# Optimization experiments

Measured on AMD Instinct MI355X. Metric: run time of the kernel, lower is better.

The kernel has to match this reference:

```python
import jax, jax.numpy as jnp
import numpy as np

ND, ED, HD, L, K = 128, 64, 256, 4, 24   # node_dim, edge_dim(num_rbf), hidden_dim, num_layers, max_neighbors
CUTOFF = 8.0
N = 2048  # n_atoms


def _silu(x):
    return x * jax.nn.sigmoid(x)


def _lattice(lengths, angles):
    a, b, c = lengths[0], lengths[1], lengths[2]
    deg = jnp.asarray(np.pi / 180.0, lengths.dtype)
    al, be, ga = angles[0] * deg, angles[1] * deg, angles[2] * deg
    lx = a
    xy = b * jnp.cos(ga)
    xz = c * jnp.cos(be)
    ly = b * jnp.sin(ga)
    yz = (b * c * jnp.cos(al) - xy * xz) / ly
    lz = jnp.sqrt(c ** 2 - xz ** 2 - yz ** 2)
    z = jnp.zeros((), lengths.dtype)
    return jnp.stack([jnp.stack([lx, z, z]), jnp.stack([xy, ly, z]), jnp.stack([xz, yz, lz])])


def _rbf(d):
    centers = jnp.linspace(0.0, CUTOFF, ED)
    widths = jnp.full((ED,), CUTOFF / ED)
    d = d[..., None]
    g = jnp.exp(-(d - centers) ** 2 / (2.0 * widths ** 2))
    cv = 0.5 * (jnp.cos(d * jnp.pi / CUTOFF) + 1.0) * (d < CUTOFF).astype(d.dtype)
    return g * cv


def _forward(atom_types, frac_coords, lengths, angles, timesteps, emb, tW, tb,
             eW1, eb1, eW2, eb2, nW1, nb1, nW2, nb2, cW1, cb1, cW2, cb2):
    n = frac_coords.shape[0]
    lattice = _lattice(lengths, angles)            # [3,3]
    cart = frac_coords @ lattice                   # [n,3]

    # ---- vectorized periodic neighbor graph (replaces host triple loop) ----
    shifts = jnp.asarray(np.array([[i, j, k] for i in (-1, 0, 1) for j in (-1, 0, 1) for k in (-1, 0, 1)],
                                  dtype=np.float32))
    sv = shifts @ lattice                          # [27,3]
    p = cart[None, :, :] + sv[:, None, :]          # [27,n,3] shifted atom positions
    # squared distances without materializing [27,n,n,3]
    d2 = (p * p).sum(-1)[:, :, None] + (cart * cart).sum(-1)[None, None, :] \
         - 2.0 * jnp.einsum('snk,mk->snm', p, cart)      # [27, n_j, n_i]
    dist = jnp.sqrt(jnp.maximum(d2, 1e-12))
    cand = jnp.where((dist < CUTOFF) & (dist > 0.01), dist, jnp.inf)
    cand = cand.reshape(27 * n, n).T               # [n_i, 27*n_j]; flat f = s*n + j
    _, idx = jax.lax.top_k(-cand, K)               # K smallest distances per atom i
    d_k = jnp.take_along_axis(cand, idx, axis=1)   # [n,K]
    dst = (idx % n).reshape(-1)                    # neighbor atom j (edge_list = [i, j])
    src = jnp.repeat(jnp.arange(n), K)             # center atom i
    valid = jnp.isfinite(d_k).reshape(-1)
    m = valid.astype(jnp.float32)[:, None]         # [E,1] pad mask
    d_e = jnp.where(valid, d_k.reshape(-1), 0.0)
    edge_attr = _rbf(d_e)                          # [E, ED]

    # ---- EGNN stack ----
    nf = emb[atom_types] + timesteps @ tW + tb     # [n, ND]
    coords = cart
    seg = lambda x, i: jax.ops.segment_sum(x, i, num_segments=n)
    for l in range(L):
        ef = jnp.concatenate([nf[src], nf[dst], edge_attr], axis=-1)   # [E, 2*ND+ED]
        msg = _silu(_silu(ef @ eW1[l] + eb1[l]) @ eW2[l] + eb2[l])     # [E, HD]
        aggr = seg(msg * m, dst)                                       # [n, HD]
        nf = nf + _silu(jnp.concatenate([nf, aggr], axis=-1) @ nW1[l] + nb1[l]) @ nW2[l] + nb2[l]
        w = _silu(msg @ cW1[l] + cb1[l]) @ cW2[l] + cb2[l]             # [E,1]
        cd = coords[src] - coords[dst]
        cd = cd / (jnp.linalg.norm(cd, axis=-1, keepdims=True) + 1e-8)
        coords = coords + seg(w * cd * m, dst)
    return nf, coords


def setup_inputs() -> dict:
    key = jax.random.key(0)
    ks = jax.random.split(key, 16)
    pr = lambda k, shape: jax.random.normal(k, shape, jnp.float32) * 0.02
    return dict(
        atom_types=jax.random.randint(ks[0], (N,), 0, 100),
        frac_coords=jax.random.uniform(ks[1], (N, 3), jnp.float32),
        lengths=jnp.ones((3,), jnp.float32) * 12.0,
        angles=jnp.ones((3,), jnp.float32) * 90.0,
        timesteps=jax.random.normal(ks[2], (N, 128), jnp.float32),
        emb=pr(ks[3], (100, ND)),
        tW=pr(ks[4], (128, ND)), tb=jnp.zeros((ND,), jnp.float32),
        eW1=pr(ks[5], (L, 2 * ND + ED, HD)), eb1=jnp.zeros((L, HD), jnp.float32),
        eW2=pr(ks[6], (L, HD, HD)), eb2=jnp.zeros((L, HD), jnp.float32),
        nW1=pr(ks[7], (L, ND + HD, HD)), nb1=jnp.zeros((L, HD), jnp.float32),
        nW2=pr(ks[8], (L, HD, ND)), nb2=jnp.zeros((L, ND), jnp.float32),
        cW1=pr(ks[9], (L, HD, HD // 2)), cb1=jnp.zeros((L, HD // 2), jnp.float32),
        cW2=pr(ks[10], (L, HD // 2, 1)), cb2=jnp.zeros((L, 1), jnp.float32),
    )


def reference(atom_types, frac_coords, lengths, angles, timesteps, emb, tW, tb,
              eW1, eb1, eW2, eb2, nW1, nb1, nW2, nb2, cW1, cb1, cW2, cb2):
    return _forward(atom_types, frac_coords, lengths, angles, timesteps, emb, tW, tb,
                    eW1, eb1, eW2, eb2, nW1, nb1, nW2, nb2, cW1, cb1, cW2, cb2)
```

## Files before the change

kernel.cpp:

```cpp
#include <hip/hip_runtime.h>
#include <math.h>

#define NA 2048
#define KN 24
#define NE (NA*KN)
#define NDIM 128
#define EDIM 64
#define HDIM 256
#define NLAYER 4
#define MAXDEG 256

typedef __attribute__((ext_vector_type(8))) short bf16x8;
typedef __attribute__((ext_vector_type(4))) float f32x4;

__device__ __forceinline__ float siluf(float x) { return x / (1.0f + expf(-x)); }
__device__ __forceinline__ ushort f2b(float x) {
    unsigned u = __float_as_uint(x);
    return (ushort)((u + 0x7fffu + ((u >> 16) & 1u)) >> 16);
}
__device__ __forceinline__ float b2f(ushort h) { return __uint_as_float(((unsigned)h) << 16); }

__device__ __forceinline__ void gl_lds(const void* g, void* lds) {
    __builtin_amdgcn_global_load_lds(
        (const __attribute__((address_space(1))) unsigned int*)g,
        (__attribute__((address_space(3))) unsigned int*)lds, 16, 0, 0);
}

struct Lat { float lx, xy, xz, ly, yz, lz; };

__device__ __forceinline__ Lat make_lattice(const float* lengths, const float* angles) {
    const float deg = 0.017453292519943295f;
    float a = lengths[0], b = lengths[1], c = lengths[2];
    float al = angles[0]*deg, be = angles[1]*deg, ga = angles[2]*deg;
    Lat L;
    L.lx = a;
    L.xy = b * cosf(ga);
    L.xz = c * cosf(be);
    L.ly = b * sinf(ga);
    L.yz = (b*c*cosf(al) - L.xy*L.xz) / L.ly;
    L.lz = sqrtf(c*c - L.xz*L.xz - L.yz*L.yz);
    return L;
}

__global__ void setup_kernel(const float* __restrict__ frac, const float* __restrict__ lengths,
                             const float* __restrict__ angles, float* __restrict__ cart,
                             float* __restrict__ cxg, float* __restrict__ cyg,
                             float* __restrict__ czg, float* __restrict__ sv) {
    int i = blockIdx.x*blockDim.x + threadIdx.x;
    Lat L = make_lattice(lengths, angles);
    if (i < NA) {
        float f0 = frac[i*3], f1 = frac[i*3+1], f2 = frac[i*3+2];
        float x = f0*L.lx + f1*L.xy + f2*L.xz;
        float y = f1*L.ly + f2*L.yz;
        float z = f2*L.lz;
        cart[i*3+0] = x; cart[i*3+1] = y; cart[i*3+2] = z;
        cxg[i] = x; cyg[i] = y; czg[i] = z;
    }
    if (i < 27) {
        float s0 = (float)(i/9 - 1), s1 = (float)((i/3)%3 - 1), s2 = (float)(i%3 - 1);
        sv[i*3+0] = s0*L.lx + s1*L.xy + s2*L.xz;
        sv[i*3+1] = s1*L.ly + s2*L.yz;
        sv[i*3+2] = s2*L.lz;
    }
}

__global__ __launch_bounds__(64) void knn_kernel(
        const float* __restrict__ cxg, const float* __restrict__ cyg,
        const float* __restrict__ czg, const float* __restrict__ lengths,
        const float* __restrict__ angles, const float* __restrict__ sv,
        int* __restrict__ dstl, ushort* __restrict__ rbf16) {
    __shared__ float sd2L[16][64];
    __shared__ int   sfL[16][64];
    const int lane = threadIdx.x;
    const int i = blockIdx.x;
    Lat L = make_lattice(lengths, angles);
    const float deg = 0.017453292519943295f;
    const bool ortho = fabsf(cosf(angles[0]*deg)) < 1e-6f &&
                       fabsf(cosf(angles[1]*deg)) < 1e-6f &&
                       fabsf(cosf(angles[2]*deg)) < 1e-6f;
    const float cx = cxg[i], cy = cyg[i], cz = czg[i];
    const float invlx = 1.0f/L.lx, invly = 1.0f/L.ly, invlz = 1.0f/L.lz;
    float R = 2.8f;
    int mycnt = 0, cnt = 0;
    bool flatm = false;
    for (int attempt = 0; attempt < 8; ++attempt) {
        const float R2 = R*R;
        mycnt = 0;
        flatm = !ortho || (attempt == 7);
        if (!flatm) {
#pragma unroll 2
            for (int j0 = 0; j0 < NA; j0 += 64) {
                const int j = j0 + lane;
                const float dx = cxg[j] - cx, dy = cyg[j] - cy, dz = czg[j] - cz;
                const float kx = rintf(dx*invlx), ky = rintf(dy*invly), kz = rintf(dz*invlz);
                const float ex = dx - (kx*L.lx + ky*L.xy + kz*L.xz);
                const float ey = dy - (ky*L.ly + kz*L.yz);
                const float ez = dz - kz*L.lz;
                const float d2 = fmaf(ex,ex,fmaf(ey,ey,ez*ez));
                if (d2 < R2 && d2 > 1e-4f) {
                    const int s = (1-(int)kx)*9 + (1-(int)ky)*3 + (1-(int)kz);
                    if (mycnt < 16) { sd2L[mycnt][lane] = d2; sfL[mycnt][lane] = (s<<11) + j; }
                    ++mycnt;
                }
            }
            if (__ballot(mycnt > 16)) {
                flatm = true;
            } else {
                int tot = mycnt;
                for (int off = 32; off > 0; off >>= 1) tot += __shfl_xor(tot, off, 64);
                cnt = tot;
            }
        }
        if (flatm) {
            cnt = 0;
            for (int s = 0; s < 27; ++s) {
                const float svx = sv[s*3], svy = sv[s*3+1], svz = sv[s*3+2];
                for (int j0 = 0; j0 < NA; j0 += 64) {
                    const int j = j0 + lane;
                    const float ex = cxg[j] + svx - cx;
                    const float ey = cyg[j] + svy - cy;
                    const float ez = czg[j] + svz - cz;
                    const float d2 = fmaf(ex,ex,fmaf(ey,ey,ez*ez));
                    const bool hit = (d2 < R2) && (d2 > 1e-4f);
                    const unsigned long long m = __ballot(hit);
                    const int rank = __popcll(m & ((1ull<<lane)-1ull));
                    const int slot = cnt + rank;
                    if (hit && slot < 1024) { sd2L[slot>>6][slot&63] = d2; sfL[slot>>6][slot&63] = (s<<11)+j; }
                    cnt += __popcll(m);
                }
            }
            cnt = min(cnt, 1024);
        }
        if (cnt >= KN) break;
        R = fminf(R*1.6f, flatm ? 8.0f : 5.9f);
    }
    int vq;
    if (flatm) vq = (lane < cnt) ? min(16, ((cnt - 1 - lane) >> 6) + 1) : 0;
    else       vq = mycnt;
    unsigned long long key[16];
#pragma unroll
    for (int q = 0; q < 16; ++q) {
        const float d2v = sd2L[q][lane];
        const int fl = sfL[q][lane];
        const unsigned long long kk = ((unsigned long long)__float_as_uint(d2v) << 20)
                                    | ((unsigned long long)(unsigned)fl << 4) | (unsigned)q;
        key[q] = (q < vq) ? kk : ~0ull;
    }
    float der[KN];
    for (int k = 0; k < KN; ++k) {
        unsigned long long lm = key[0];
#pragma unroll
        for (int q = 1; q < 16; ++q) lm = key[q] < lm ? key[q] : lm;
        for (int off = 32; off > 0; off >>= 1) {
            unsigned long long o = __shfl_xor(lm, off, 64);
            lm = o < lm ? o : lm;
        }
        der[k] = sqrtf(__uint_as_float((unsigned)(lm >> 20)));
        if (lane == 0) dstl[i*KN + k] = (int)((lm >> 4) & 2047u);
#pragma unroll
        for (int q = 0; q < 16; ++q) if (key[q] == lm) key[q] = ~0ull;
    }
    const float center = (8.0f/63.0f) * (float)lane;
    for (int k = 0; k < KN; ++k) {
        const float d = der[k];
        const float diff = d - center;
        const float g = expf(diff*diff * -32.0f);
        const float cv = 0.5f * (cosf(d * (float)(M_PI/8.0)) + 1.0f);
        rbf16[(size_t)(i*KN + k)*EDIM + lane] = f2b(g * cv);
    }
}

__global__ void scatter_kernel(const int* __restrict__ dstl, int* __restrict__ ccnt,
                               int* __restrict__ cedg) {
    int e = blockIdx.x*256 + threadIdx.x;
    if (e >= NE) return;
    int j = dstl[e];
    int slot = atomicAdd(&ccnt[j], 1);
    if (slot < MAXDEG) cedg[(size_t)j*MAXDEG + slot] = e;
}

__global__ void csort_kernel(const int* __restrict__ ccnt, int* __restrict__ cedg) {
    const int j = blockIdx.x*4 + (threadIdx.x >> 6);
    const int lane = threadIdx.x & 63;
    const int cnt = min(ccnt[j], MAXDEG);
    if (cnt <= 64) {
        int v = (lane < cnt) ? cedg[(size_t)j*MAXDEG + lane] : 0x7FFFFFFF;
#pragma unroll
        for (int k = 2; k <= 64; k <<= 1) {
#pragma unroll
            for (int s = k >> 1; s > 0; s >>= 1) {
                int o = __shfl_xor(v, s, 64);
                const bool up = ((lane & k) == 0);
                const bool lowhalf = ((lane & s) == 0);
                v = ((lowhalf == up) ? min(v, o) : max(v, o));
            }
        }
        if (lane < cnt) cedg[(size_t)j*MAXDEG + lane] = v;
    } else if (lane == 0) {
        int* L = cedg + (size_t)j*MAXDEG;
        for (int a = 1; a < cnt; ++a) {
            int v = L[a]; int b = a - 1;
            while (b >= 0 && L[b] > v) { L[b+1] = L[b]; --b; }
            L[b+1] = v;
        }
    }
}

__global__ void nf_init_kernel(const int* __restrict__ atom_types, const float* __restrict__ ts,
                               const float* __restrict__ emb, const float* __restrict__ tW,
                               const float* __restrict__ tb, float* __restrict__ nf,
                               ushort* __restrict__ nf16) {
    int i = blockIdx.x, c = threadIdx.x;
    float acc = emb[atom_types[i]*NDIM + c] + tb[c];
    for (int kk = 0; kk < 128; ++kk) acc += ts[i*128 + kk] * tW[kk*NDIM + c];
    nf[i*NDIM + c] = acc;
    nf16[i*NDIM + c] = f2b(acc);
}

__global__ void wprep_all(const float* __restrict__ eW1, const float* __restrict__ eW2,
                          const float* __restrict__ cW1, const float* __restrict__ nW1,
                          const float* __restrict__ nW2,
                          ushort* __restrict__ eW1t, ushort* __restrict__ eW2t,
                          ushort* __restrict__ cW1t, ushort* __restrict__ nW1t,
                          ushort* __restrict__ nW2t) {
    __shared__ float tile[64][65];
    const int b = blockIdx.x;
    const float* W; ushort* Wt; int Kk, Nn, rel;
    if (b < 80)       { W = eW1; Wt = eW1t; Kk = 320; Nn = 256; rel = b; }
    else if (b < 144) { W = eW2; Wt = eW2t; Kk = 256; Nn = 256; rel = b - 80; }
    else if (b < 176) { W = cW1; Wt = cW1t; Kk = 256; Nn = 128; rel = b - 144; }
    else if (b < 272) { W = nW1; Wt = nW1t; Kk = 384; Nn = 256; rel = b - 176; }
    else              { W = nW2; Wt = nW2t; Kk = 256; Nn = 128; rel = b - 272; }
    const int kt = Kk >> 6, nt = Nn >> 6, per = kt*nt;
    const int l = rel / per, r2 = rel - l*per;
    const int k0 = (r2 / nt) * 64, n0 = (r2 - (r2/nt)*nt) * 64;
    const float* Wl = W + (size_t)l*Kk*Nn;
    ushort* Wtl = Wt + (size_t)l*Kk*Nn;
    const int tr = threadIdx.x >> 6, tc = threadIdx.x & 63;
#pragma unroll
    for (int q = 0; q < 16; ++q) {
        const int k = q*4 + tr;
        tile[k][tc] = Wl[(size_t)(k0 + k)*Nn + n0 + tc];
    }
    __syncthreads();
#pragma unroll
    for (int q = 0; q < 16; ++q) {
        const int n = q*4 + tr;
        Wtl[(size_t)(n0 + n)*Kk + k0 + tc] = f2b(tile[tc][n]);
    }
}

template<int AMODE, int EPI>
__global__ __launch_bounds__(256) void bgemm_kernel(
        const ushort* __restrict__ A, const ushort* __restrict__ nf16,
        const int* __restrict__ dstl, const ushort* __restrict__ rbf16,
        const ushort* __restrict__ aggr16, const ushort* __restrict__ Bt,
        const float* __restrict__ bias, const float* __restrict__ res,
        const float* __restrict__ cW2v, const float* __restrict__ cb2v,
        float* __restrict__ wvout,
        float* __restrict__ Cf, ushort* __restrict__ C16, int M, int Nn, int Kk) {
    __shared__ alignas(16) ushort As[2][128*32];
    __shared__ alignas(16) ushort Bs[2][128*32];
    __shared__ int sdst[128];
    const int t = threadIdx.x;
    const int wave = t >> 6, lane = t & 63;
    const int row0 = blockIdx.x*128, col0 = blockIdx.y*128;
    if (AMODE == 1) {
        if (t < 128) sdst[t] = dstl[row0 + t];
        __syncthreads();
    }
    const int wr = (wave >> 1)*64, wc = (wave & 1)*64;
    const int lr = lane & 15, g0 = lane >> 4;

    auto STAGE = [&](int buf, int k0) {
#pragma unroll
        for (int q = 0; q < 4; ++q) {
            const int rbase = (q & 1)*64 + wave*16;
            const int r = rbase + (lane >> 2);
            const int g = (lane & 3) ^ ((r >> 1) & 3);
            const int kg = k0 + g*8;
            const int ldsbase = rbase * 32;
            if (q < 2) {
                const ushort* gp;
                if (AMODE == 0) {
                    gp = A + (size_t)(row0 + r)*Kk + kg;
                } else if (AMODE == 1) {
                    const int e = row0 + r;
                    if (kg < NDIM)        gp = nf16 + (size_t)(e/KN)*NDIM + kg;
                    else if (kg < 2*NDIM) gp = nf16 + (size_t)sdst[r]*NDIM + (kg - NDIM);
                    else                  gp = rbf16 + (size_t)e*EDIM + (kg - 2*NDIM);
                } else {
                    const int e = row0 + r;
                    if (kg < NDIM) gp = nf16 + (size_t)e*NDIM + kg;
                    else           gp = aggr16 + (size_t)e*HDIM + (kg - NDIM);
                }
                gl_lds(gp, &As[buf][ldsbase]);
            } else {
                gl_lds(Bt + (size_t)(col0 + r)*Kk + kg, &Bs[buf][ldsbase]);
            }
        }
    };

    f32x4 acc[4][4] = {};
    const int nk = Kk >> 5;
    STAGE(0, 0);
    int cur = 0;
    for (int it = 0; it < nk; ++it) {
        if (it + 1 < nk) {
            STAGE(cur ^ 1, (it + 1) << 5);
            asm volatile("s_waitcnt vmcnt(4)" ::: "memory");
        } else {
            asm volatile("s_waitcnt vmcnt(0)" ::: "memory");
        }
        __builtin_amdgcn_sched_barrier(0);
        __builtin_amdgcn_s_barrier();
        __builtin_amdgcn_sched_barrier(0);
        bf16x8 af[4], bfr[4];
#pragma unroll
        for (int m = 0; m < 4; ++m) {
            const int rA = wr + m*16 + lr;
            af[m] = *reinterpret_cast<const bf16x8*>(&As[cur][rA*32 + (g0 ^ ((rA>>1)&3))*8]);
        }
#pragma unroll
        for (int n = 0; n < 4; ++n) {
            const int rB = wc + n*16 + lr;
            bfr[n] = *reinterpret_cast<const bf16x8*>(&Bs[cur][rB*32 + (g0 ^ ((rB>>1)&3))*8]);
        }
#pragma unroll
        for (int m = 0; m < 4; ++m)
#pragma unroll
            for (int n = 0; n < 4; ++n)
                acc[m][n] = __builtin_amdgcn_mfma_f32_16x16x32_bf16(af[m], bfr[n], acc[m][n], 0, 0, 0);
        asm volatile("s_waitcnt lgkmcnt(0)" ::: "memory");
        __builtin_amdgcn_sched_barrier(0);
        __builtin_amdgcn_s_barrier();
        __builtin_amdgcn_sched_barrier(0);
        cur ^= 1;
    }

    if constexpr (EPI == 3) {
        __shared__ float wred[2][128];
        float part[4][4];
#pragma unroll
        for (int m = 0; m < 4; ++m)
#pragma unroll
            for (int j = 0; j < 4; ++j) part[m][j] = 0.0f;
#pragma unroll
        for (int n = 0; n < 4; ++n) {
            const int cc = wc + n*16 + lr;
            const float bb = bias[cc];
            const float cw = cW2v[cc];
#pragma unroll
            for (int m = 0; m < 4; ++m)
#pragma unroll
                for (int j = 0; j < 4; ++j)
                    part[m][j] += siluf(acc[m][n][j] + bb) * cw;
        }
#pragma unroll
        for (int off = 1; off < 16; off <<= 1)
#pragma unroll
            for (int m = 0; m < 4; ++m)
#pragma unroll
                for (int j = 0; j < 4; ++j)
                    part[m][j] += __shfl_xor(part[m][j], off, 64);
        if (lr == 0) {
#pragma unroll
            for (int m = 0; m < 4; ++m)
#pragma unroll
                for (int j = 0; j < 4; ++j)
                    wred[wave & 1][wr + m*16 + g0*4 + j] = part[m][j];
        }
        __syncthreads();
        if (t < 128) wvout[row0 + t] = wred[0][t] + wred[1][t] + cb2v[0];
        return;
    }

#pragma unroll
    for (int n = 0; n < 4; ++n) {
        const int cc = col0 + wc + n*16 + lr;
        const float bb = bias[cc];
#pragma unroll
        for (int m = 0; m < 4; ++m) {
#pragma unroll
            for (int j = 0; j < 4; ++j) {
                const int rr = row0 + wr + m*16 + (lane >> 4)*4 + j;
                float x = acc[m][n][j] + bb;
                if constexpr (EPI == 0) {
                    C16[(size_t)rr*Nn + cc] = f2b(siluf(x));
                } else {
                    x += res[(size_t)rr*Nn + cc];
                    Cf[(size_t)rr*Nn + cc] = x;
                    C16[(size_t)rr*Nn + cc] = f2b(x);
                }
            }
        }
    }
}

__global__ void aggr_kernel(const ushort* __restrict__ msg16, const int* __restrict__ ccnt,
                            const int* __restrict__ cedg, ushort* __restrict__ aggr16) {
    __shared__ int se[4][64];
    const int w = threadIdx.x >> 6, lane = threadIdx.x & 63;
    const int j = blockIdx.x*4 + w;
    const int cnt = min(ccnt[j], MAXDEG);
    se[w][lane] = (lane < cnt) ? cedg[(size_t)j*MAXDEG + lane] : 0;
    __syncthreads();
    const int c4 = lane*4;
    float s0 = 0, s1 = 0, s2 = 0, s3 = 0;
    const int lim = min(cnt, 64);
    for (int q = 0; q < lim; ++q) {
        const int e = se[w][q];
        ushort4 v = *reinterpret_cast<const ushort4*>(&msg16[(size_t)e*HDIM + c4]);
        s0 += b2f(v.x); s1 += b2f(v.y); s2 += b2f(v.z); s3 += b2f(v.w);
    }
    for (int q = 64; q < cnt; ++q) {
        const int e = cedg[(size_t)j*MAXDEG + q];
        ushort4 v = *reinterpret_cast<const ushort4*>(&msg16[(size_t)e*HDIM + c4]);
        s0 += b2f(v.x); s1 += b2f(v.y); s2 += b2f(v.z); s3 += b2f(v.w);
    }
    ushort4 o; o.x = f2b(s0); o.y = f2b(s1); o.z = f2b(s2); o.w = f2b(s3);
    *reinterpret_cast<ushort4*>(&aggr16[(size_t)j*HDIM + c4]) = o;
}

__global__ void coords_kernel(const float* __restrict__ cold, const float* __restrict__ wv,
                              const int* __restrict__ ccnt, const int* __restrict__ cedg,
                              float* __restrict__ cnew) {
    const int w = threadIdx.x >> 6, lane = threadIdx.x & 63;
    const int j = blockIdx.x*4 + w;
    const int cnt = min(ccnt[j], MAXDEG);
    const float jx = cold[j*3], jy = cold[j*3+1], jz = cold[j*3+2];
    float dx = 0, dy = 0, dz = 0;
    for (int q = lane; q < cnt; q += 64) {
        const int e = cedg[(size_t)j*MAXDEG + q];
        const int si = e / KN;
        const float ax = cold[si*3]   - jx;
        const float ay = cold[si*3+1] - jy;
        const float az = cold[si*3+2] - jz;
        const float inv = wv[e] / (sqrtf(ax*ax + ay*ay + az*az) + 1e-8f);
        dx += inv*ax; dy += inv*ay; dz += inv*az;
    }
    for (int off = 32; off > 0; off >>= 1) {
        dx += __shfl_xor(dx, off, 64);
        dy += __shfl_xor(dy, off, 64);
        dz += __shfl_xor(dz, off, 64);
    }
    if (lane == 0) {
        cnew[j*3]   = jx + dx;
        cnew[j*3+1] = jy + dy;
        cnew[j*3+2] = jz + dz;
    }
}

__global__ void copyout_kernel(const float* __restrict__ nf, const float* __restrict__ coords,
                               float* __restrict__ out) {
    int idx = blockIdx.x*256 + threadIdx.x;
    if (idx < NA*NDIM) out[idx] = nf[idx];
    else if (idx < NA*NDIM + NA*3) out[idx] = coords[idx - NA*NDIM];
}

extern "C" void kernel_launch(void* const* d_in, const int* in_sizes, int n_in,
                              void* d_out, int out_size, void* d_ws, size_t ws_size,
                              hipStream_t stream) {
    const int*   atom_types = (const int*)  d_in[0];
    const float* frac       = (const float*)d_in[1];
    const float* lengths    = (const float*)d_in[2];
    const float* angles     = (const float*)d_in[3];
    const float* timesteps  = (const float*)d_in[4];
    const float* emb        = (const float*)d_in[5];
    const float* tW         = (const float*)d_in[6];
    const float* tb         = (const float*)d_in[7];
    const float* eW1        = (const float*)d_in[8];
    const float* eb1        = (const float*)d_in[9];
    const float* eW2        = (const float*)d_in[10];
    const float* eb2        = (const float*)d_in[11];
    const float* nW1        = (const float*)d_in[12];
    const float* nb1        = (const float*)d_in[13];
    const float* nW2        = (const float*)d_in[14];
    const float* nb2        = (const float*)d_in[15];
    const float* cW1        = (const float*)d_in[16];
    const float* cb1        = (const float*)d_in[17];
    const float* cW2        = (const float*)d_in[18];
    const float* cb2        = (const float*)d_in[19];

    char* p = (char*)d_ws;
    auto alloc = [&](size_t bytes) { char* q = p; p += (bytes + 255) & ~(size_t)255; return q; };
    float*  sv    = (float*) alloc(81*4);
    float*  c0    = (float*) alloc((size_t)NA*3*4);
    float*  c1    = (float*) alloc((size_t)NA*3*4);
    float*  cxg   = (float*) alloc((size_t)NA*4);
    float*  cyg   = (float*) alloc((size_t)NA*4);
    float*  czg   = (float*) alloc((size_t)NA*4);
    float*  nf    = (float*) alloc((size_t)NA*NDIM*4);
    int*    dstl  = (int*)   alloc((size_t)NE*4);
    ushort* rbf16 = (ushort*)alloc((size_t)NE*EDIM*2);
    int*    ccnt  = (int*)   alloc((size_t)NA*4);
    int*    cedg  = (int*)   alloc((size_t)NA*MAXDEG*4);
    ushort* aggr16= (ushort*)alloc((size_t)NA*HDIM*2);
    ushort* t116  = (ushort*)alloc((size_t)NA*HDIM*2);
    float*  wv    = (float*) alloc((size_t)NE*4);
    ushort* nf16  = (ushort*)alloc((size_t)NA*NDIM*2);
    ushort* h116  = (ushort*)alloc((size_t)NE*HDIM*2);
    ushort* msg16 = (ushort*)alloc((size_t)NE*HDIM*2);
    ushort* eW1t  = (ushort*)alloc((size_t)NLAYER*(2*NDIM+EDIM)*HDIM*2);
    ushort* eW2t  = (ushort*)alloc((size_t)NLAYER*HDIM*HDIM*2);
    ushort* cW1t  = (ushort*)alloc((size_t)NLAYER*(HDIM/2)*HDIM*2);
    ushort* nW1t  = (ushort*)alloc((size_t)NLAYER*(NDIM+HDIM)*HDIM*2);
    ushort* nW2t  = (ushort*)alloc((size_t)NLAYER*HDIM*NDIM*2);

    setup_kernel<<<8, 256, 0, stream>>>(frac, lengths, angles, c0, cxg, cyg, czg, sv);
    knn_kernel<<<NA, 64, 0, stream>>>(cxg, cyg, czg, lengths, angles, sv, dstl, rbf16);
    hipMemsetAsync(ccnt, 0, (size_t)NA*4, stream);
    scatter_kernel<<<NE/256, 256, 0, stream>>>(dstl, ccnt, cedg);
    csort_kernel<<<NA/4, 256, 0, stream>>>(ccnt, cedg);
    nf_init_kernel<<<NA, 128, 0, stream>>>(atom_types, timesteps, emb, tW, tb, nf, nf16);
    wprep_all<<<304, 256, 0, stream>>>(eW1, eW2, cW1, nW1, nW2, eW1t, eW2t, cW1t, nW1t, nW2t);

    float* cin = c0; float* cout = c1;
    for (int l = 0; l < NLAYER; ++l) {
        const float* eb1l = eb1 + (size_t)l*HDIM;
        const float* eb2l = eb2 + (size_t)l*HDIM;
        const float* nb1l = nb1 + (size_t)l*HDIM;
        const float* nb2l = nb2 + (size_t)l*NDIM;
        const float* cb1l = cb1 + (size_t)l*(HDIM/2);
        const float* cW2l = cW2 + (size_t)l*(HDIM/2);
        const float* cb2l = cb2 + (size_t)l;

        bgemm_kernel<1,0><<<dim3(NE/128, HDIM/128), 256, 0, stream>>>(
            nullptr, nf16, dstl, rbf16, nullptr, eW1t + (size_t)l*(2*NDIM+EDIM)*HDIM, eb1l,
            nullptr, nullptr, nullptr, nullptr, nullptr, h116, NE, HDIM, 2*NDIM+EDIM);
        bgemm_kernel<0,0><<<dim3(NE/128, HDIM/128), 256, 0, stream>>>(
            h116, nullptr, nullptr, nullptr, nullptr, eW2t + (size_t)l*HDIM*HDIM, eb2l,
            nullptr, nullptr, nullptr, nullptr, nullptr, msg16, NE, HDIM, HDIM);
        aggr_kernel<<<NA/4, 256, 0, stream>>>(msg16, ccnt, cedg, aggr16);
        bgemm_kernel<2,0><<<dim3(NA/128, HDIM/128), 256, 0, stream>>>(
            nullptr, nf16, nullptr, nullptr, aggr16, nW1t + (size_t)l*(NDIM+HDIM)*HDIM, nb1l,
            nullptr, nullptr, nullptr, nullptr, nullptr, t116, NA, HDIM, NDIM+HDIM);
        bgemm_kernel<0,2><<<dim3(NA/128, NDIM/128), 256, 0, stream>>>(
            t116, nullptr, nullptr, nullptr, nullptr, nW2t + (size_t)l*HDIM*NDIM, nb2l,
            nf, nullptr, nullptr, nullptr, nf, nf16, NA, NDIM, HDIM);
        bgemm_kernel<0,3><<<dim3(NE/128, 1), 256, 0, stream>>>(
            msg16, nullptr, nullptr, nullptr, nullptr, cW1t + (size_t)l*(HDIM/2)*HDIM, cb1l,
            nullptr, cW2l, cb2l, wv, nullptr, nullptr, NE, HDIM/2, HDIM);
        coords_kernel<<<NA/4, 256, 0, stream>>>(cin, wv, ccnt, cedg, cout);
        float* tmp = cin; cin = cout; cout = tmp;
    }
    copyout_kernel<<<(NA*NDIM + NA*3)/256, 256, 0, stream>>>(nf, cin, (float*)d_out);
}
```

Measured before the change: 436.6 us.

## Factor edge MLP first layer per node and fuse edge MLP chain into one kernel

The first edge-MLP layer's source and destination node projections are now computed once per atom as a node-level GEMM, giving a 2048x512 table P16, instead of once per edge over 49k rows. Only the RBF part (K=64) is multiplied per edge. A new fused edge_kernel gathers the per-node projections, applies SiLU, runs the second edge GEMM, writes the messages, and computes the coordinate weight head. Each edge tile is held in LDS between stages, which removes the h1 round trip through global memory and the separate coordinate-head launch. The cost is heavy LDS use per block, which lowers occupancy, plus added rounding because the node projections are stored in bf16 before the sum.

```diff
diff --git a/kernel.cpp b/kernel.cpp
--- a/kernel.cpp
+++ b/kernel.cpp
@@ -220,22 +220,37 @@
 __global__ void wprep_all(const float* __restrict__ eW1, const float* __restrict__ eW2,
                           const float* __restrict__ cW1, const float* __restrict__ nW1,
                           const float* __restrict__ nW2,
-                          ushort* __restrict__ eW1t, ushort* __restrict__ eW2t,
-                          ushort* __restrict__ cW1t, ushort* __restrict__ nW1t,
-                          ushort* __restrict__ nW2t) {
+                          ushort* __restrict__ eW1abt, ushort* __restrict__ eW1ct,
+                          ushort* __restrict__ eW2t, ushort* __restrict__ cW1t,
+                          ushort* __restrict__ nW1t, ushort* __restrict__ nW2t) {
     __shared__ float tile[64][65];
     const int b = blockIdx.x;
-    const float* W; ushort* Wt; int Kk, Nn, rel;
-    if (b < 80)       { W = eW1; Wt = eW1t; Kk = 320; Nn = 256; rel = b; }
-    else if (b < 144) { W = eW2; Wt = eW2t; Kk = 256; Nn = 256; rel = b - 80; }
-    else if (b < 176) { W = cW1; Wt = cW1t; Kk = 256; Nn = 128; rel = b - 144; }
-    else if (b < 272) { W = nW1; Wt = nW1t; Kk = 384; Nn = 256; rel = b - 176; }
-    else              { W = nW2; Wt = nW2t; Kk = 256; Nn = 128; rel = b - 272; }
-    const int kt = Kk >> 6, nt = Nn >> 6, per = kt*nt;
-    const int l = rel / per, r2 = rel - l*per;
-    const int k0 = (r2 / nt) * 64, n0 = (r2 - (r2/nt)*nt) * 64;
-    const float* Wl = W + (size_t)l*Kk*Nn;
-    ushort* Wtl = Wt + (size_t)l*Kk*Nn;
+    int l, kt, nt, Kk, Nn, Kd, n0d, k0d;
+    const float* Wl; ushort* Wd;
+    if (b < 80) {
+        int rel = b; l = rel/20; int r = rel%20; kt = r/4; nt = r%4;
+        Kk = 320; Nn = 256; Wl = eW1 + (size_t)l*Kk*Nn;
+        if (kt < 2)      { Wd = eW1abt + (size_t)l*512*128; Kd = 128; n0d = nt*64;       k0d = kt*64; }
+        else if (kt < 4) { Wd = eW1abt + (size_t)l*512*128; Kd = 128; n0d = nt*64 + 256; k0d = (kt-2)*64; }
+        else             { Wd = eW1ct  + (size_t)l*256*64;  Kd = 64;  n0d = nt*64;       k0d = 0; }
+    } else if (b < 144) {
+        int rel = b-80; l = rel/16; int r = rel%16; kt = r/4; nt = r%4;
+        Kk = 256; Nn = 256; Wl = eW2 + (size_t)l*Kk*Nn; Wd = eW2t + (size_t)l*Kk*Nn;
+        Kd = 256; n0d = nt*64; k0d = kt*64;
+    } else if (b < 176) {
+        int rel = b-144; l = rel/8; int r = rel%8; kt = r/2; nt = r%2;
+        Kk = 256; Nn = 128; Wl = cW1 + (size_t)l*Kk*Nn; Wd = cW1t + (size_t)l*Kk*Nn;
+        Kd = 256; n0d = nt*64; k0d = kt*64;
+    } else if (b < 272) {
+        int rel = b-176; l = rel/24; int r = rel%24; kt = r/4; nt = r%4;
+        Kk = 384; Nn = 256; Wl = nW1 + (size_t)l*Kk*Nn; Wd = nW1t + (size_t)l*Kk*Nn;
+        Kd = 384; n0d = nt*64; k0d = kt*64;
+    } else {
+        int rel = b-272; l = rel/8; int r = rel%8; kt = r/2; nt = r%2;
+        Kk = 256; Nn = 128; Wl = nW2 + (size_t)l*Kk*Nn; Wd = nW2t + (size_t)l*Kk*Nn;
+        Kd = 256; n0d = nt*64; k0d = kt*64;
+    }
+    const int k0 = kt*64, n0 = nt*64;
     const int tr = threadIdx.x >> 6, tc = threadIdx.x & 63;
 #pragma unroll
     for (int q = 0; q < 16; ++q) {
@@ -246,29 +261,21 @@
 #pragma unroll
     for (int q = 0; q < 16; ++q) {
         const int n = q*4 + tr;
-        Wtl[(size_t)(n0 + n)*Kk + k0 + tc] = f2b(tile[tc][n]);
+        Wd[(size_t)(n0d + n)*Kd + k0d + tc] = f2b(tile[tc][n]);
     }
 }
 
 template<int AMODE, int EPI>
 __global__ __launch_bounds__(256) void bgemm_kernel(
         const ushort* __restrict__ A, const ushort* __restrict__ nf16,
-        const int* __restrict__ dstl, const ushort* __restrict__ rbf16,
         const ushort* __restrict__ aggr16, const ushort* __restrict__ Bt,
         const float* __restrict__ bias, const float* __restrict__ res,
-        const float* __restrict__ cW2v, const float* __restrict__ cb2v,
-        float* __restrict__ wvout,
         float* __restrict__ Cf, ushort* __restrict__ C16, int M, int Nn, int Kk) {
     __shared__ alignas(16) ushort As[2][128*32];
     __shared__ alignas(16) ushort Bs[2][128*32];
-    __shared__ int sdst[128];
     const int t = threadIdx.x;
     const int wave = t >> 6, lane = t & 63;
     const int row0 = blockIdx.x*128, col0 = blockIdx.y*128;
-    if (AMODE == 1) {
-        if (t < 128) sdst[t] = dstl[row0 + t];
-        __syncthreads();
-    }
     const int wr = (wave >> 1)*64, wc = (wave & 1)*64;
     const int lr = lane & 15, g0 = lane >> 4;
 
@@ -284,11 +291,6 @@
                 const ushort* gp;
                 if (AMODE == 0) {
                     gp = A + (size_t)(row0 + r)*Kk + kg;
-                } else if (AMODE == 1) {
-                    const int e = row0 + r;
-                    if (kg < NDIM)        gp = nf16 + (size_t)(e/KN)*NDIM + kg;
-                    else if (kg < 2*NDIM) gp = nf16 + (size_t)sdst[r]*NDIM + (kg - NDIM);
-                    else                  gp = rbf16 + (size_t)e*EDIM + (kg - 2*NDIM);
                 } else {
                     const int e = row0 + r;
                     if (kg < NDIM) gp = nf16 + (size_t)e*NDIM + kg;
@@ -338,47 +340,10 @@
         cur ^= 1;
     }
 
-    if constexpr (EPI == 3) {
-        __shared__ float wred[2][128];
-        float part[4][4];
-#pragma unroll
-        for (int m = 0; m < 4; ++m)
-#pragma unroll
-            for (int j = 0; j < 4; ++j) part[m][j] = 0.0f;
-#pragma unroll
-        for (int n = 0; n < 4; ++n) {
-            const int cc = wc + n*16 + lr;
-            const float bb = bias[cc];
-            const float cw = cW2v[cc];
-#pragma unroll
-            for (int m = 0; m < 4; ++m)
-#pragma unroll
-                for (int j = 0; j < 4; ++j)
-                    part[m][j] += siluf(acc[m][n][j] + bb) * cw;
-        }
-#pragma unroll
-        for (int off = 1; off < 16; off <<= 1)
-#pragma unroll
-            for (int m = 0; m < 4; ++m)
-#pragma unroll
-                for (int j = 0; j < 4; ++j)
-                    part[m][j] += __shfl_xor(part[m][j], off, 64);
-        if (lr == 0) {
-#pragma unroll
-            for (int m = 0; m < 4; ++m)
-#pragma unroll
-                for (int j = 0; j < 4; ++j)
-                    wred[wave & 1][wr + m*16 + g0*4 + j] = part[m][j];
-        }
-        __syncthreads();
-        if (t < 128) wvout[row0 + t] = wred[0][t] + wred[1][t] + cb2v[0];
-        return;
-    }
-
 #pragma unroll
     for (int n = 0; n < 4; ++n) {
         const int cc = col0 + wc + n*16 + lr;
-        const float bb = bias[cc];
+        const float bb = (EPI == 1) ? 0.0f : bias[cc];
 #pragma unroll
         for (int m = 0; m < 4; ++m) {
 #pragma unroll
@@ -387,6 +352,8 @@
                 float x = acc[m][n][j] + bb;
                 if constexpr (EPI == 0) {
                     C16[(size_t)rr*Nn + cc] = f2b(siluf(x));
+                } else if constexpr (EPI == 1) {
+                    C16[(size_t)rr*Nn + cc] = f2b(x);
                 } else {
                     x += res[(size_t)rr*Nn + cc];
                     Cf[(size_t)rr*Nn + cc] = x;
@@ -395,6 +362,265 @@
             }
         }
     }
+}
+
+__global__ __launch_bounds__(256) void edge_kernel(
+        const ushort* __restrict__ P16,
+        const int* __restrict__ dstl,
+        const ushort* __restrict__ rbf16,
+        const ushort* __restrict__ W1ct,
+        const ushort* __restrict__ W2t,
+        const ushort* __restrict__ cW1t,
+        const float* __restrict__ eb1, const float* __restrict__ eb2,
+        const float* __restrict__ cb1, const float* __restrict__ cW2v,
+        const float* __restrict__ cb2v,
+        ushort* __restrict__ msg16, float* __restrict__ wvout) {
+    __shared__ alignas(16) ushort Hs[128*256];
+    __shared__ alignas(16) ushort Ps[8*272];
+    __shared__ alignas(16) char U[49152];
+    __shared__ int sdst[128];
+    __shared__ float wred[2][128];
+    ushort* Rb = (ushort*)U;
+    ushort* Wc = (ushort*)(U + 16384);
+    ushort* Bs = (ushort*)U;
+    ushort* Cs = (ushort*)(U + 32768);
+
+    const int t = threadIdx.x, wave = t >> 6, lane = t & 63;
+    const int row0 = blockIdx.x*128;
+    const int src0 = row0 / KN;
+    if (t < 128) sdst[t] = dstl[row0 + t];
+    __syncthreads();
+
+    const int wr = (wave >> 1)*64;
+    const int wcB = (wave & 1)*128;
+    const int lr = lane & 15, g0 = lane >> 4;
+
+#pragma unroll
+    for (int q = 0; q < 16; ++q) {
+        const int base = wave*16384 + q*1024;
+        const int r = (base >> 9) + (lane >> 5);
+        const int cp = lane & 31;
+        const int g = cp ^ ((r & 7) << 2);
+        gl_lds(P16 + (size_t)sdst[r]*512 + 256 + g*8, (char*)Hs + base);
+    }
+#pragma unroll
+    for (int q = 0; q < 4; ++q) {
+        const int base = wave*4096 + q*1024;
+        const int r = (base >> 7) + (lane >> 3);
+        const int g = (lane & 7) ^ (r & 7);
+        gl_lds(rbf16 + (size_t)(row0 + r)*64 + g*8, (char*)Rb + base);
+    }
+#pragma unroll
+    for (int q = 0; q < 8; ++q) {
+        const int base = wave*8192 + q*1024;
+        const int n = (base >> 7) + (lane >> 3);
+        const int g = (lane & 7) ^ (n & 7);
+        gl_lds(W1ct + (size_t)n*64 + g*8, (char*)Wc + base);
+    }
+    {
+        const int rid = t >> 5, cp = t & 31;
+        const int srow = min(src0 + rid, NA - 1);
+        uint4 v = *reinterpret_cast<const uint4*>(P16 + (size_t)srow*512 + cp*8);
+        *reinterpret_cast<uint4*>(&Ps[rid*272 + cp*8]) = v;
+    }
+    __syncthreads();
+
+    f32x4 acc[4][8];
+#pragma unroll
+    for (int m = 0; m < 4; ++m)
+#pragma unroll
+        for (int n = 0; n < 8; ++n) acc[m][n] = (f32x4){0.f,0.f,0.f,0.f};
+#pragma unroll
+    for (int ks = 0; ks < 2; ++ks) {
+        bf16x8 af[4], bfr[8];
+#pragma unroll
+        for (int m = 0; m < 4; ++m) {
+            const int rA = wr + m*16 + lr;
+            af[m] = *reinterpret_cast<const bf16x8*>(&Rb[rA*64 + ((ks*4 + g0) ^ (rA & 7))*8]);
+        }
+#pragma unroll
+        for (int n = 0; n < 8; ++n) {
+            const int rB = wcB + n*16 + lr;
+            bfr[n] = *reinterpret_cast<const bf16x8*>(&Wc[rB*64 + ((ks*4 + g0) ^ (rB & 7))*8]);
+        }
+#pragma unroll
+        for (int m = 0; m < 4; ++m)
+#pragma unroll
+            for (int n = 0; n < 8; ++n)
+                acc[m][n] = __builtin_amdgcn_mfma_f32_16x16x32_bf16(af[m], bfr[n], acc[m][n], 0, 0, 0);
+    }
+#pragma unroll
+    for (int n = 0; n < 8; ++n) {
+        const int cc = wcB + n*16 + lr;
+        const float b1 = eb1[cc];
+#pragma unroll
+        for (int m = 0; m < 4; ++m) {
+#pragma unroll
+            for (int j = 0; j < 4; ++j) {
+                const int rr = wr + m*16 + g0*4 + j;
+                const int srel = (row0 + rr)/KN - src0;
+                const float ps = b2f(Ps[srel*272 + cc]);
+                const int hoff = rr*256 + (((cc>>3) ^ ((rr&7)<<2))*8) + (cc&7);
+                const float pd = b2f(Hs[hoff]);
+                Hs[hoff] = f2b(siluf(acc[m][n][j] + ps + pd + b1));
+            }
+        }
+    }
+    __syncthreads();
+
+#pragma unroll
+    for (int m = 0; m < 4; ++m)
+#pragma unroll
+        for (int n = 0; n < 8; ++n) acc[m][n] = (f32x4){0.f,0.f,0.f,0.f};
+    auto STAGEB = [&](int buf, int k0) {
+#pragma unroll
+        for (int q = 0; q < 4; ++q) {
+            const int loc = wave*4096 + q*1024;
+            const int n = (loc >> 6) + (lane >> 2);
+            const int g = (lane & 3) ^ ((n >> 1) & 3);
+            gl_lds(W2t + (size_t)n*256 + k0 + g*8, (char*)Bs + buf*16384 + loc);
+        }
+    };
+    int cur = 0;
+    STAGEB(0, 0);
+    for (int it = 0; it < 8; ++it) {
+        if (it + 1 < 8) {
+            STAGEB(cur ^ 1, (it + 1)*32);
+            asm volatile("s_waitcnt vmcnt(4)" ::: "memory");
+        } else {
+            asm volatile("s_waitcnt vmcnt(0)" ::: "memory");
+        }
+        __builtin_amdgcn_sched_barrier(0);
+        __builtin_amdgcn_s_barrier();
+        __builtin_amdgcn_sched_barrier(0);
+        bf16x8 af[4], bfr[8];
+#pragma unroll
+        for (int m = 0; m < 4; ++m) {
+            const int rA = wr + m*16 + lr;
+            af[m] = *reinterpret_cast<const bf16x8*>(&Hs[rA*256 + (((it*4 + g0) ^ ((rA&7)<<2))*8)]);
+        }
+#pragma unroll
+        for (int n = 0; n < 8; ++n) {
+            const int rB = wcB + n*16 + lr;
+            bfr[n] = *reinterpret_cast<const bf16x8*>(&Bs[(size_t)cur*8192 + rB*32 + (g0 ^ ((rB>>1)&3))*8]);
+        }
+#pragma unroll
+        for (int m = 0; m < 4; ++m)
+#pragma unroll
+            for (int n = 0; n < 8; ++n)
+                acc[m][n] = __builtin_amdgcn_mfma_f32_16x16x32_bf16(af[m], bfr[n], acc[m][n], 0, 0, 0);
+        asm volatile("s_waitcnt lgkmcnt(0)" ::: "memory");
+        __builtin_amdgcn_sched_barrier(0);
+        __builtin_amdgcn_s_barrier();
+        __builtin_amdgcn_sched_barrier(0);
+        cur ^= 1;
+    }
+#pragma unroll
+    for (int n = 0; n < 8; ++n) {
+        const int cc = wcB + n*16 + lr;
+        const float b2 = eb2[cc];
+#pragma unroll
+        for (int m = 0; m < 4; ++m) {
+#pragma unroll
+            for (int j = 0; j < 4; ++j) {
+                const int rr = wr + m*16 + g0*4 + j;
+                const int hoff = rr*256 + (((cc>>3) ^ ((rr&7)<<2))*8) + (cc&7);
+                Hs[hoff] = f2b(siluf(acc[m][n][j] + b2));
+            }
+        }
+    }
+    __syncthreads();
+#pragma unroll
+    for (int q = 0; q < 16; ++q) {
+        const int off = wave*16384 + q*1024 + lane*16;
+        const int r = off >> 9;
+        const int cp = (off >> 4) & 31;
+        const int g = cp ^ ((r & 7) << 2);
+        uint4 v = *reinterpret_cast<const uint4*>((const char*)Hs + off);
+        *reinterpret_cast<uint4*>(msg16 + (size_t)(row0 + r)*256 + g*8) = v;
+    }
+
+    const int wcC = (wave & 1)*64;
+    f32x4 acc3[4][4];
+#pragma unroll
+    for (int m = 0; m < 4; ++m)
+#pragma unroll
+        for (int n = 0; n < 4; ++n) acc3[m][n] = (f32x4){0.f,0.f,0.f,0.f};
+    auto STAGEC = [&](int buf, int k0) {
+#pragma unroll
+        for (int q = 0; q < 2; ++q) {
+            const int loc = wave*2048 + q*1024;
+            const int n = (loc >> 6) + (lane >> 2);
+            const int g = (lane & 3) ^ ((n >> 1) & 3);
+            gl_lds(cW1t + (size_t)n*256 + k0 + g*8, (char*)Cs + buf*8192 + loc);
+        }
+    };
+    cur = 0;
+    STAGEC(0, 0);
+    for (int it = 0; it < 8; ++it) {
+        if (it + 1 < 8) {
+            STAGEC(cur ^ 1, (it + 1)*32);
+            asm volatile("s_waitcnt vmcnt(2)" ::: "memory");
+        } else {
+            asm volatile("s_waitcnt vmcnt(0)" ::: "memory");
+        }
+        __builtin_amdgcn_sched_barrier(0);
+        __builtin_amdgcn_s_barrier();
+        __builtin_amdgcn_sched_barrier(0);
+        bf16x8 af[4], bfr[4];
+#pragma unroll
+        for (int m = 0; m < 4; ++m) {
+            const int rA = wr + m*16 + lr;
+            af[m] = *reinterpret_cast<const bf16x8*>(&Hs[rA*256 + (((it*4 + g0) ^ ((rA&7)<<2))*8)]);
+        }
+#pragma unroll
+        for (int n = 0; n < 4; ++n) {
+            const int rB = wcC + n*16 + lr;
+            bfr[n] = *reinterpret_cast<const bf16x8*>(&Cs[(size_t)cur*4096 + rB*32 + (g0 ^ ((rB>>1)&3))*8]);
+        }
+#pragma unroll
+        for (int m = 0; m < 4; ++m)
+#pragma unroll
+            for (int n = 0; n < 4; ++n)
+                acc3[m][n] = __builtin_amdgcn_mfma_f32_16x16x32_bf16(af[m], bfr[n], acc3[m][n], 0, 0, 0);
+        asm volatile("s_waitcnt lgkmcnt(0)" ::: "memory");
+        __builtin_amdgcn_sched_barrier(0);
+        __builtin_amdgcn_s_barrier();
+        __builtin_amdgcn_sched_barrier(0);
+        cur ^= 1;
+    }
+    float part[4][4];
+#pragma unroll
+    for (int m = 0; m < 4; ++m)
+#pragma unroll
+        for (int j = 0; j < 4; ++j) part[m][j] = 0.0f;
+#pragma unroll
+    for (int n = 0; n < 4; ++n) {
+        const int cc = wcC + n*16 + lr;
+        const float bb = cb1[cc];
+        const float cw = cW2v[cc];
+#pragma unroll
+        for (int m = 0; m < 4; ++m)
+#pragma unroll
+            for (int j = 0; j < 4; ++j)
+                part[m][j] += siluf(acc3[m][n][j] + bb) * cw;
+    }
+#pragma unroll
+    for (int off = 1; off < 16; off <<= 1)
+#pragma unroll
+        for (int m = 0; m < 4; ++m)
+#pragma unroll
+            for (int j = 0; j < 4; ++j)
+                part[m][j] += __shfl_xor(part[m][j], off, 64);
+    if (lr == 0) {
+#pragma unroll
+        for (int m = 0; m < 4; ++m)
+#pragma unroll
+            for (int j = 0; j < 4; ++j)
+                wred[wave & 1][wr + m*16 + g0*4 + j] = part[m][j];
+    }
+    __syncthreads();
+    if (t < 128) wvout[row0 + t] = wred[0][t] + wred[1][t] + cb2v[0];
 }
 
 __global__ void aggr_kernel(const ushort* __restrict__ msg16, const int* __restrict__ ccnt,
@@ -499,9 +725,10 @@
     ushort* t116  = (ushort*)alloc((size_t)NA*HDIM*2);
     float*  wv    = (float*) alloc((size_t)NE*4);
     ushort* nf16  = (ushort*)alloc((size_t)NA*NDIM*2);
-    ushort* h116  = (ushort*)alloc((size_t)NE*HDIM*2);
+    ushort* P16   = (ushort*)alloc((size_t)NA*512*2);
     ushort* msg16 = (ushort*)alloc((size_t)NE*HDIM*2);
-    ushort* eW1t  = (ushort*)alloc((size_t)NLAYER*(2*NDIM+EDIM)*HDIM*2);
+    ushort* eW1abt= (ushort*)alloc((size_t)NLAYER*512*128*2);
+    ushort* eW1ct = (ushort*)alloc((size_t)NLAYER*256*64*2);
     ushort* eW2t  = (ushort*)alloc((size_t)NLAYER*HDIM*HDIM*2);
     ushort* cW1t  = (ushort*)alloc((size_t)NLAYER*(HDIM/2)*HDIM*2);
     ushort* nW1t  = (ushort*)alloc((size_t)NLAYER*(NDIM+HDIM)*HDIM*2);
@@ -513,7 +740,8 @@
     scatter_kernel<<<NE/256, 256, 0, stream>>>(dstl, ccnt, cedg);
     csort_kernel<<<NA/4, 256, 0, stream>>>(ccnt, cedg);
     nf_init_kernel<<<NA, 128, 0, stream>>>(atom_types, timesteps, emb, tW, tb, nf, nf16);
-    wprep_all<<<304, 256, 0, stream>>>(eW1, eW2, cW1, nW1, nW2, eW1t, eW2t, cW1t, nW1t, nW2t);
+    wprep_all<<<304, 256, 0, stream>>>(eW1, eW2, cW1, nW1, nW2,
+                                       eW1abt, eW1ct, eW2t, cW1t, nW1t, nW2t);
 
     float* cin = c0; float* cout = c1;
     for (int l = 0; l < NLAYER; ++l) {
@@ -525,22 +753,19 @@
         const float* cW2l = cW2 + (size_t)l*(HDIM/2);
         const float* cb2l = cb2 + (size_t)l;
 
-        bgemm_kernel<1,0><<<dim3(NE/128, HDIM/128), 256, 0, stream>>>(
-            nullptr, nf16, dstl, rbf16, nullptr, eW1t + (size_t)l*(2*NDIM+EDIM)*HDIM, eb1l,
-            nullptr, nullptr, nullptr, nullptr, nullptr, h116, NE, HDIM, 2*NDIM+EDIM);
-        bgemm_kernel<0,0><<<dim3(NE/128, HDIM/128), 256, 0, stream>>>(
-            h116, nullptr, nullptr, nullptr, nullptr, eW2t + (size_t)l*HDIM*HDIM, eb2l,
-            nullptr, nullptr, nullptr, nullptr, nullptr, msg16, NE, HDIM, HDIM);
+        bgemm_kernel<0,1><<<dim3(16, 4), 256, 0, stream>>>(
+            nf16, nullptr, nullptr, eW1abt + (size_t)l*512*128, nullptr, nullptr,
+            nullptr, P16, NA, 512, 128);
+        edge_kernel<<<NE/128, 256, 0, stream>>>(
+            P16, dstl, rbf16, eW1ct + (size_t)l*256*64, eW2t + (size_t)l*HDIM*HDIM,
+            cW1t + (size_t)l*(HDIM/2)*HDIM, eb1l, eb2l, cb1l, cW2l, cb2l, msg16, wv);
         aggr_kernel<<<NA/4, 256, 0, stream>>>(msg16, ccnt, cedg, aggr16);
         bgemm_kernel<2,0><<<dim3(NA/128, HDIM/128), 256, 0, stream>>>(
-            nullptr, nf16, nullptr, nullptr, aggr16, nW1t + (size_t)l*(NDIM+HDIM)*HDIM, nb1l,
-            nullptr, nullptr, nullptr, nullptr, nullptr, t116, NA, HDIM, NDIM+HDIM);
+            nullptr, nf16, aggr16, nW1t + (size_t)l*(NDIM+HDIM)*HDIM, nb1l, nullptr,
+            nullptr, t116, NA, HDIM, NDIM+HDIM);
         bgemm_kernel<0,2><<<dim3(NA/128, NDIM/128), 256, 0, stream>>>(
-            t116, nullptr, nullptr, nullptr, nullptr, nW2t + (size_t)l*HDIM*NDIM, nb2l,
-            nf, nullptr, nullptr, nullptr, nf, nf16, NA, NDIM, HDIM);
-        bgemm_kernel<0,3><<<dim3(NE/128, 1), 256, 0, stream>>>(
-            msg16, nullptr, nullptr, nullptr, nullptr, cW1t + (size_t)l*(HDIM/2)*HDIM, cb1l,
-            nullptr, cW2l, cb2l, wv, nullptr, nullptr, NE, HDIM/2, HDIM);
+            t116, nullptr, nullptr, nW2t + (size_t)l*HDIM*NDIM, nb2l, nf,
+            nf, nf16, NA, NDIM, HDIM);
         coords_kernel<<<NA/4, 256, 0, stream>>>(cin, wv, ccnt, cedg, cout);
         float* tmp = cin; cin = cout; cout = tmp;
     }
```

Measured after the change: 540.5 us. 1.24x slower.

## Factor edge-MLP first layer into per-node projections plus RBF GEMM

Applied to the files above, without the earlier changes.

The first edge-MLP layer multiplies the concatenation [nf_src, nf_dst, rbf] by eW1. That product is now split: a node-level GEMM projects nf through the src and dst blocks of eW1 into a per-node table P16, and the edge GEMM only multiplies the 64-wide RBF features. P16 rows are gathered and added in the epilogue before SiLU. This cuts the edge GEMM's K from 320 to 64 and removes the gathered A loads. The cost is an extra launch, scattered bf16 epilogue loads, and an extra bf16 rounding of the partial sums.

```diff
diff --git a/kernel.cpp b/kernel.cpp
--- a/kernel.cpp
+++ b/kernel.cpp
@@ -220,22 +220,37 @@
 __global__ void wprep_all(const float* __restrict__ eW1, const float* __restrict__ eW2,
                           const float* __restrict__ cW1, const float* __restrict__ nW1,
                           const float* __restrict__ nW2,
-                          ushort* __restrict__ eW1t, ushort* __restrict__ eW2t,
-                          ushort* __restrict__ cW1t, ushort* __restrict__ nW1t,
-                          ushort* __restrict__ nW2t) {
+                          ushort* __restrict__ eW1abt, ushort* __restrict__ eW1ct,
+                          ushort* __restrict__ eW2t, ushort* __restrict__ cW1t,
+                          ushort* __restrict__ nW1t, ushort* __restrict__ nW2t) {
     __shared__ float tile[64][65];
     const int b = blockIdx.x;
-    const float* W; ushort* Wt; int Kk, Nn, rel;
-    if (b < 80)       { W = eW1; Wt = eW1t; Kk = 320; Nn = 256; rel = b; }
-    else if (b < 144) { W = eW2; Wt = eW2t; Kk = 256; Nn = 256; rel = b - 80; }
-    else if (b < 176) { W = cW1; Wt = cW1t; Kk = 256; Nn = 128; rel = b - 144; }
-    else if (b < 272) { W = nW1; Wt = nW1t; Kk = 384; Nn = 256; rel = b - 176; }
-    else              { W = nW2; Wt = nW2t; Kk = 256; Nn = 128; rel = b - 272; }
-    const int kt = Kk >> 6, nt = Nn >> 6, per = kt*nt;
-    const int l = rel / per, r2 = rel - l*per;
-    const int k0 = (r2 / nt) * 64, n0 = (r2 - (r2/nt)*nt) * 64;
-    const float* Wl = W + (size_t)l*Kk*Nn;
-    ushort* Wtl = Wt + (size_t)l*Kk*Nn;
+    int l, kt, nt, Kk, Nn, Kd, n0d, k0d;
+    const float* Wl; ushort* Wd;
+    if (b < 80) {
+        int rel = b; l = rel/20; int r = rel%20; kt = r/4; nt = r%4;
+        Kk = 320; Nn = 256; Wl = eW1 + (size_t)l*Kk*Nn;
+        if (kt < 2)      { Wd = eW1abt + (size_t)l*512*128; Kd = 128; n0d = nt*64;       k0d = kt*64; }
+        else if (kt < 4) { Wd = eW1abt + (size_t)l*512*128; Kd = 128; n0d = nt*64 + 256; k0d = (kt-2)*64; }
+        else             { Wd = eW1ct  + (size_t)l*256*64;  Kd = 64;  n0d = nt*64;       k0d = 0; }
+    } else if (b < 144) {
+        int rel = b-80; l = rel/16; int r = rel%16; kt = r/4; nt = r%4;
+        Kk = 256; Nn = 256; Wl = eW2 + (size_t)l*Kk*Nn; Wd = eW2t + (size_t)l*Kk*Nn;
+        Kd = 256; n0d = nt*64; k0d = kt*64;
+    } else if (b < 176) {
+        int rel = b-144; l = rel/8; int r = rel%8; kt = r/2; nt = r%2;
+        Kk = 256; Nn = 128; Wl = cW1 + (size_t)l*Kk*Nn; Wd = cW1t + (size_t)l*Kk*Nn;
+        Kd = 256; n0d = nt*64; k0d = kt*64;
+    } else if (b < 272) {
+        int rel = b-176; l = rel/24; int r = rel%24; kt = r/4; nt = r%4;
+        Kk = 384; Nn = 256; Wl = nW1 + (size_t)l*Kk*Nn; Wd = nW1t + (size_t)l*Kk*Nn;
+        Kd = 384; n0d = nt*64; k0d = kt*64;
+    } else {
+        int rel = b-272; l = rel/8; int r = rel%8; kt = r/2; nt = r%2;
+        Kk = 256; Nn = 128; Wl = nW2 + (size_t)l*Kk*Nn; Wd = nW2t + (size_t)l*Kk*Nn;
+        Kd = 256; n0d = nt*64; k0d = kt*64;
+    }
+    const int k0 = kt*64, n0 = nt*64;
     const int tr = threadIdx.x >> 6, tc = threadIdx.x & 63;
 #pragma unroll
     for (int q = 0; q < 16; ++q) {
@@ -246,15 +261,15 @@
 #pragma unroll
     for (int q = 0; q < 16; ++q) {
         const int n = q*4 + tr;
-        Wtl[(size_t)(n0 + n)*Kk + k0 + tc] = f2b(tile[tc][n]);
+        Wd[(size_t)(n0d + n)*Kd + k0d + tc] = f2b(tile[tc][n]);
     }
 }
 
 template<int AMODE, int EPI>
 __global__ __launch_bounds__(256) void bgemm_kernel(
         const ushort* __restrict__ A, const ushort* __restrict__ nf16,
-        const int* __restrict__ dstl, const ushort* __restrict__ rbf16,
-        const ushort* __restrict__ aggr16, const ushort* __restrict__ Bt,
+        const ushort* __restrict__ aggr16, const int* __restrict__ dstl,
+        const ushort* __restrict__ P16, const ushort* __restrict__ Bt,
         const float* __restrict__ bias, const float* __restrict__ res,
         const float* __restrict__ cW2v, const float* __restrict__ cb2v,
         float* __restrict__ wvout,
@@ -265,7 +280,7 @@
     const int t = threadIdx.x;
     const int wave = t >> 6, lane = t & 63;
     const int row0 = blockIdx.x*128, col0 = blockIdx.y*128;
-    if (AMODE == 1) {
+    if (EPI == 4) {
         if (t < 128) sdst[t] = dstl[row0 + t];
         __syncthreads();
     }
@@ -284,11 +299,6 @@
                 const ushort* gp;
                 if (AMODE == 0) {
                     gp = A + (size_t)(row0 + r)*Kk + kg;
-                } else if (AMODE == 1) {
-                    const int e = row0 + r;
-                    if (kg < NDIM)        gp = nf16 + (size_t)(e/KN)*NDIM + kg;
-                    else if (kg < 2*NDIM) gp = nf16 + (size_t)sdst[r]*NDIM + (kg - NDIM);
-                    else                  gp = rbf16 + (size_t)e*EDIM + (kg - 2*NDIM);
                 } else {
                     const int e = row0 + r;
                     if (kg < NDIM) gp = nf16 + (size_t)e*NDIM + kg;
@@ -378,7 +388,7 @@
 #pragma unroll
     for (int n = 0; n < 4; ++n) {
         const int cc = col0 + wc + n*16 + lr;
-        const float bb = bias[cc];
+        const float bb = (EPI == 1) ? 0.0f : bias[cc];
 #pragma unroll
         for (int m = 0; m < 4; ++m) {
 #pragma unroll
@@ -387,10 +397,18 @@
                 float x = acc[m][n][j] + bb;
                 if constexpr (EPI == 0) {
                     C16[(size_t)rr*Nn + cc] = f2b(siluf(x));
-                } else {
+                } else if constexpr (EPI == 1) {
+                    C16[(size_t)rr*Nn + cc] = f2b(x);
+                } else if constexpr (EPI == 2) {
                     x += res[(size_t)rr*Nn + cc];
                     Cf[(size_t)rr*Nn + cc] = x;
                     C16[(size_t)rr*Nn + cc] = f2b(x);
+                } else {
+                    const int srci = rr / KN;
+                    const int dstj = sdst[rr - row0];
+                    x += b2f(P16[(size_t)srci*512 + cc]);
+                    x += b2f(P16[(size_t)dstj*512 + 256 + cc]);
+                    C16[(size_t)rr*Nn + cc] = f2b(siluf(x));
                 }
             }
         }
@@ -499,9 +517,11 @@
     ushort* t116  = (ushort*)alloc((size_t)NA*HDIM*2);
     float*  wv    = (float*) alloc((size_t)NE*4);
     ushort* nf16  = (ushort*)alloc((size_t)NA*NDIM*2);
+    ushort* P16   = (ushort*)alloc((size_t)NA*512*2);
     ushort* h116  = (ushort*)alloc((size_t)NE*HDIM*2);
     ushort* msg16 = (ushort*)alloc((size_t)NE*HDIM*2);
-    ushort* eW1t  = (ushort*)alloc((size_t)NLAYER*(2*NDIM+EDIM)*HDIM*2);
+    ushort* eW1abt= (ushort*)alloc((size_t)NLAYER*512*128*2);
+    ushort* eW1ct = (ushort*)alloc((size_t)NLAYER*256*64*2);
     ushort* eW2t  = (ushort*)alloc((size_t)NLAYER*HDIM*HDIM*2);
     ushort* cW1t  = (ushort*)alloc((size_t)NLAYER*(HDIM/2)*HDIM*2);
     ushort* nW1t  = (ushort*)alloc((size_t)NLAYER*(NDIM+HDIM)*HDIM*2);
@@ -513,7 +533,8 @@
     scatter_kernel<<<NE/256, 256, 0, stream>>>(dstl, ccnt, cedg);
     csort_kernel<<<NA/4, 256, 0, stream>>>(ccnt, cedg);
     nf_init_kernel<<<NA, 128, 0, stream>>>(atom_types, timesteps, emb, tW, tb, nf, nf16);
-    wprep_all<<<304, 256, 0, stream>>>(eW1, eW2, cW1, nW1, nW2, eW1t, eW2t, cW1t, nW1t, nW2t);
+    wprep_all<<<304, 256, 0, stream>>>(eW1, eW2, cW1, nW1, nW2,
+                                       eW1abt, eW1ct, eW2t, cW1t, nW1t, nW2t);
 
     float* cin = c0; float* cout = c1;
     for (int l = 0; l < NLAYER; ++l) {
@@ -525,22 +546,25 @@
         const float* cW2l = cW2 + (size_t)l*(HDIM/2);
         const float* cb2l = cb2 + (size_t)l;
 
-        bgemm_kernel<1,0><<<dim3(NE/128, HDIM/128), 256, 0, stream>>>(
-            nullptr, nf16, dstl, rbf16, nullptr, eW1t + (size_t)l*(2*NDIM+EDIM)*HDIM, eb1l,
-            nullptr, nullptr, nullptr, nullptr, nullptr, h116, NE, HDIM, 2*NDIM+EDIM);
+        bgemm_kernel<0,1><<<dim3(NA/128, 4), 256, 0, stream>>>(
+            nf16, nullptr, nullptr, nullptr, nullptr, eW1abt + (size_t)l*512*128,
+            nullptr, nullptr, nullptr, nullptr, nullptr, nullptr, P16, NA, 512, 128);
+        bgemm_kernel<0,4><<<dim3(NE/128, HDIM/128), 256, 0, stream>>>(
+            rbf16, nullptr, nullptr, dstl, P16, eW1ct + (size_t)l*256*64,
+            eb1l, nullptr, nullptr, nullptr, nullptr, nullptr, h116, NE, HDIM, EDIM);
         bgemm_kernel<0,0><<<dim3(NE/128, HDIM/128), 256, 0, stream>>>(
-            h116, nullptr, nullptr, nullptr, nullptr, eW2t + (size_t)l*HDIM*HDIM, eb2l,
-            nullptr, nullptr, nullptr, nullptr, nullptr, msg16, NE, HDIM, HDIM);
+            h116, nullptr, nullptr, nullptr, nullptr, eW2t + (size_t)l*HDIM*HDIM,
+            eb2l, nullptr, nullptr, nullptr, nullptr, nullptr, msg16, NE, HDIM, HDIM);
         aggr_kernel<<<NA/4, 256, 0, stream>>>(msg16, ccnt, cedg, aggr16);
         bgemm_kernel<2,0><<<dim3(NA/128, HDIM/128), 256, 0, stream>>>(
-            nullptr, nf16, nullptr, nullptr, aggr16, nW1t + (size_t)l*(NDIM+HDIM)*HDIM, nb1l,
-            nullptr, nullptr, nullptr, nullptr, nullptr, t116, NA, HDIM, NDIM+HDIM);
+            nullptr, nf16, aggr16, nullptr, nullptr, nW1t + (size_t)l*(NDIM+HDIM)*HDIM,
+            nb1l, nullptr, nullptr, nullptr, nullptr, nullptr, t116, NA, HDIM, NDIM+HDIM);
         bgemm_kernel<0,2><<<dim3(NA/128, NDIM/128), 256, 0, stream>>>(
-            t116, nullptr, nullptr, nullptr, nullptr, nW2t + (size_t)l*HDIM*NDIM, nb2l,
-            nf, nullptr, nullptr, nullptr, nf, nf16, NA, NDIM, HDIM);
+            t116, nullptr, nullptr, nullptr, nullptr, nW2t + (size_t)l*HDIM*NDIM,
+            nb2l, nf, nullptr, nullptr, nullptr, nf, nf16, NA, NDIM, HDIM);
         bgemm_kernel<0,3><<<dim3(NE/128, 1), 256, 0, stream>>>(
-            msg16, nullptr, nullptr, nullptr, nullptr, cW1t + (size_t)l*(HDIM/2)*HDIM, cb1l,
-            nullptr, cW2l, cb2l, wv, nullptr, nullptr, NE, HDIM/2, HDIM);
+            msg16, nullptr, nullptr, nullptr, nullptr, cW1t + (size_t)l*(HDIM/2)*HDIM,
+            cb1l, nullptr, cW2l, cb2l, wv, nullptr, nullptr, NE, HDIM/2, HDIM);
         coords_kernel<<<NA/4, 256, 0, stream>>>(cin, wv, ccnt, cedg, cout);
         float* tmp = cin; cin = cout; cout = tmp;
     }
```

New measurement: 455.7 us. 1.04x slower.
